# Optimization experiments

Measured on AMD Instinct MI355X. Metric: run time of the kernel, lower is better.

Reference implementation:

```python
import jax, jax.numpy as jnp
import numpy as np

B, H, S, D = 2, 16, 2048, 64
SCALE = D ** -0.5  # head_dim^-0.5 with dim=1024, num_heads=16


def setup_inputs() -> dict:
    key = jax.random.key(0)
    kq, kk, kv = jax.random.split(key, 3)
    q = jax.random.normal(kq, (B, H, S, D), dtype=jnp.float32)
    k = jax.random.normal(kk, (B, H, S, D), dtype=jnp.float32)
    v = jax.random.normal(kv, (B, H, S, D), dtype=jnp.float32)
    # causal mask, broadcastable over batch and heads; 0 -> masked
    mask = jnp.tril(jnp.ones((S, S), dtype=jnp.int32))[None, None]
    return {"q": q, "k": k, "v": v, "mask": mask}


def reference(q, k, v, mask):
    # scores: [B, H, S, S]
    scores = jnp.einsum("bhqd,bhkd->bhqk", q, k) * SCALE
    scores = jnp.where(mask == 0, jnp.float32(-jnp.inf), scores)
    attn_weights = jax.nn.softmax(scores, axis=-1)
    # dropout p=0 / eval mode -> identity
    attn_output = jnp.einsum("bhqk,bhkd->bhqd", attn_weights, v)
    return attn_output, attn_weights
```

## Files before the change

kernel.cpp:

```cpp
#include <hip/hip_runtime.h>


#define S_LEN 2048
#define HD 64
#define NHEADS 32
#define NQT 32
#define ATT_SCALE 0.125f

typedef __bf16 bf16x8 __attribute__((ext_vector_type(8)));
typedef unsigned short u16x8 __attribute__((ext_vector_type(8)));
typedef float f32x4 __attribute__((ext_vector_type(4)));

__device__ __forceinline__ unsigned short f2bf(float f) {
  unsigned int u = __builtin_bit_cast(unsigned int, f);
  u += 0x7fffu + ((u >> 16) & 1u);
  return (unsigned short)(u >> 16);
}
__device__ __forceinline__ bf16x8 frag16(const unsigned short* p) {
  uint4 u = *reinterpret_cast<const uint4*>(p);
  return __builtin_bit_cast(bf16x8, u);
}
__device__ __forceinline__ bf16x8 cvt8(const float* p) {
  const float4 a = *reinterpret_cast<const float4*>(p);
  const float4 b = *reinterpret_cast<const float4*>(p + 4);
  u16x8 r;
  r[0] = f2bf(a.x); r[1] = f2bf(a.y); r[2] = f2bf(a.z); r[3] = f2bf(a.w);
  r[4] = f2bf(b.x); r[5] = f2bf(b.y); r[6] = f2bf(b.z); r[7] = f2bf(b.w);
  return __builtin_bit_cast(bf16x8, r);
}
__device__ __forceinline__ bf16x8 load8(const void* base, size_t off, bool isf32) {
  if (isf32) return cvt8(reinterpret_cast<const float*>(base) + off);
  return frag16(reinterpret_cast<const unsigned short*>(base) + off);
}
__device__ __forceinline__ bool sniff_f32(const void* q) {
  const int lane = threadIdx.x & 63;
  const unsigned int w = reinterpret_cast<const unsigned int*>(q)[lane];
  const unsigned int le = (w >> 7) & 0xFFu;
  const bool okb = (le == 0u) || (le >= 100u && le <= 140u);
  return __popcll(__ballot(okb)) < 32;
}

__global__ __launch_bounds__(256) void prep_kernel(
    const void* __restrict__ q, const void* __restrict__ k, const void* __restrict__ v,
    unsigned short* __restrict__ wq, unsigned short* __restrict__ wk,
    unsigned short* __restrict__ wv) {
  __shared__ __align__(16) unsigned short T[HD][72];
  const int tid = threadIdx.x;
  if (blockIdx.x >= 1024) {
    const bool isf32 = sniff_f32(q);
    const size_t i = ((size_t)(blockIdx.x - 1024) * 256 + tid) * 8;
    bf16x8 a = load8(q, i, isf32);
    *reinterpret_cast<uint4*>(wq + i) = __builtin_bit_cast(uint4, a);
    bf16x8 b = load8(k, i, isf32);
    *reinterpret_cast<uint4*>(wk + i) = __builtin_bit_cast(uint4, b);
    return;
  }
  const bool isf32 = sniff_f32(v);
  const int head = blockIdx.x & (NHEADS - 1);
  const int tt = blockIdx.x >> 5;
  const int r = tid >> 2;
  const int dc = (tid & 3) << 4;
  const size_t off = ((size_t)head * S_LEN + (tt << 6) + r) * HD + dc;
  const bf16x8 x0 = load8(v, off, isf32);
  const bf16x8 x1 = load8(v, off + 8, isf32);
  const u16x8 e0 = __builtin_bit_cast(u16x8, x0);
  const u16x8 e1 = __builtin_bit_cast(u16x8, x1);
#pragma unroll
  for (int e = 0; e < 8; ++e) { T[dc + e][r] = e0[e]; T[dc + 8 + e][r] = e1[e]; }
  __syncthreads();
  const int d = tid >> 2;
  const int tc = (tid & 3) << 4;
  const uint4 o0 = *reinterpret_cast<const uint4*>(&T[d][tc]);
  const uint4 o1 = *reinterpret_cast<const uint4*>(&T[d][tc + 8]);
  unsigned short* dst = wv + ((size_t)head * HD + d) * S_LEN + (tt << 6) + tc;
  *reinterpret_cast<uint4*>(dst) = o0;
  *reinterpret_cast<uint4*>(dst + 8) = o1;
}

template <bool WS>
__global__ __launch_bounds__(256, 4) void attn_kernel(
    const void* __restrict__ q, const void* __restrict__ kk, const void* __restrict__ vv,
    const unsigned short* __restrict__ wq, const unsigned short* __restrict__ wk,
    const unsigned short* __restrict__ wv,
    float* __restrict__ out_o, float* __restrict__ out_w) {
  __shared__ __align__(16) unsigned short Vt[2][HD * 72];
  __shared__ __align__(16) unsigned short Pt[4][16 * 72];

  const int blk = blockIdx.x;
  const int head = blk & (NHEADS - 1);
  const int qt = (NQT - 1) - (blk >> 5);
  const int tid = threadIdx.x;
  const int lane = tid & 63;
  const int wave = tid >> 6;
  const int q0 = qt << 6;
  const int r0 = q0 + (wave << 4);
  const int l15 = lane & 15;
  const int quad = lane >> 4;

  bool isf32 = true;
  if constexpr (!WS) isf32 = sniff_f32(q);

  const size_t qb = (size_t)head * S_LEN * HD;
  float* Wh = out_w + (size_t)head * S_LEN * S_LEN;

  {
    const int c0 = (qt + 1) << 6;
    const int nz4 = (S_LEN - c0) >> 2;
    const int row = tid >> 2;
    const f32x4 z = {0.f, 0.f, 0.f, 0.f};
    f32x4* wrow = reinterpret_cast<f32x4*>(Wh + (size_t)(q0 + row) * S_LEN + c0);
    for (int c = tid & 3; c < nz4; c += 4) __builtin_nontemporal_store(z, wrow + c);
  }

  const size_t qoff = qb + (size_t)(r0 + l15) * HD + (quad << 3);
  bf16x8 qa0, qa1;
  if constexpr (WS) { qa0 = frag16(wq + qoff); qa1 = frag16(wq + qoff + 32); }
  else              { qa0 = load8(q, qoff, isf32); qa1 = load8(q, qoff + 32, isf32); }

  auto ldk = [&](int kt, int f) -> bf16x8 {
    const size_t o = qb + (size_t)((kt << 6) + ((f >> 1) << 4) + l15) * HD +
                     (quad << 3) + ((f & 1) << 5);
    if constexpr (WS) return frag16(wk + o);
    else return load8(kk, o, isf32);
  };

  bf16x8 kc[8], kn[8];

  float lsum[4] = {0.f, 0.f, 0.f, 0.f};
#pragma unroll
  for (int f = 0; f < 8; ++f) kc[f] = ldk(0, f);
  for (int kt = 0; kt <= qt; ++kt) {
    if (kt < qt) {
#pragma unroll
      for (int f = 0; f < 8; ++f) kn[f] = ldk(kt + 1, f);
    }
    if (kt == qt) {
#pragma unroll
      for (int nc = 0; nc < 4; ++nc) {
        f32x4 acc = {0.f, 0.f, 0.f, 0.f};
        acc = __builtin_amdgcn_mfma_f32_16x16x32_bf16(qa0, kc[2 * nc], acc, 0, 0, 0);
        acc = __builtin_amdgcn_mfma_f32_16x16x32_bf16(qa1, kc[2 * nc + 1], acc, 0, 0, 0);
        const int ki = (kt << 6) + (nc << 4) + l15;
#pragma unroll
        for (int r = 0; r < 4; ++r) {
          const int qi = r0 + (quad << 2) + r;
          lsum[r] += (ki <= qi) ? __expf(acc[r] * ATT_SCALE) : 0.f;
        }
      }
    } else {
#pragma unroll
      for (int nc = 0; nc < 4; ++nc) {
        f32x4 acc = {0.f, 0.f, 0.f, 0.f};
        acc = __builtin_amdgcn_mfma_f32_16x16x32_bf16(qa0, kc[2 * nc], acc, 0, 0, 0);
        acc = __builtin_amdgcn_mfma_f32_16x16x32_bf16(qa1, kc[2 * nc + 1], acc, 0, 0, 0);
#pragma unroll
        for (int r = 0; r < 4; ++r) lsum[r] += __expf(acc[r] * ATT_SCALE);
      }
#pragma unroll
      for (int f = 0; f < 8; ++f) kc[f] = kn[f];
    }
  }
  float inv_l[4];
#pragma unroll
  for (int r = 0; r < 4; ++r) {
    float s = lsum[r];
    s += __shfl_xor(s, 1);
    s += __shfl_xor(s, 2);
    s += __shfl_xor(s, 4);
    s += __shfl_xor(s, 8);
    inv_l[r] = 1.0f / s;
  }

  const f32x4 vzero = {0.f, 0.f, 0.f, 0.f};
  f32x4 oacc[4] = {vzero, vzero, vzero, vzero};
  unsigned short* Pw = &Pt[wave][0];

  const int vd1 = tid >> 3, vtb1 = tid & 7;
  const int vd2 = (tid + 256) >> 3, vtb2 = tid & 7;
  const unsigned short* wvh = wv + (size_t)head * HD * S_LEN;
  const int ftr1 = tid >> 3, fdc = (tid & 7) << 3;
  const int ftr2 = (tid + 256) >> 3;

  uint4 va0, va1;
  bf16x8 fv0, fv1;

  auto vload = [&](int kt) {
    if constexpr (WS) {
      const unsigned short* b = wvh + (kt << 6);
      va0 = *reinterpret_cast<const uint4*>(b + (size_t)vd1 * S_LEN + (vtb1 << 3));
      va1 = *reinterpret_cast<const uint4*>(b + (size_t)vd2 * S_LEN + (vtb2 << 3));
    } else {
      fv0 = load8(vv, qb + (size_t)((kt << 6) + ftr1) * HD + fdc, isf32);
      fv1 = load8(vv, qb + (size_t)((kt << 6) + ftr2) * HD + fdc, isf32);
    }
  };
  auto vstage = [&](int buf) {
    if constexpr (WS) {
      *reinterpret_cast<uint4*>(&Vt[buf][vd1 * 72 + ((vtb1 ^ (vd1 >> 3)) << 3)]) = va0;
      *reinterpret_cast<uint4*>(&Vt[buf][vd2 * 72 + ((vtb2 ^ (vd2 >> 3)) << 3)]) = va1;
    } else {
      const u16x8 s0 = __builtin_bit_cast(u16x8, fv0);
      const u16x8 s1 = __builtin_bit_cast(u16x8, fv1);
      const int tb1 = ftr1 >> 3, tl1 = ftr1 & 7;
      const int tb2 = ftr2 >> 3, tl2 = ftr2 & 7;
#pragma unroll
      for (int e = 0; e < 8; ++e) {
        const int d = fdc + e;
        Vt[buf][d * 72 + (((tb1 ^ (d >> 3)) << 3) | tl1)] = s0[e];
        Vt[buf][d * 72 + (((tb2 ^ (d >> 3)) << 3) | tl2)] = s1[e];
      }
    }
  };

#pragma unroll
  for (int f = 0; f < 8; ++f) kc[f] = ldk(0, f);
  vload(0);
  vstage(0);
  __syncthreads();

  for (int kt = 0; kt <= qt; ++kt) {
    const bool last = (kt == qt);
    if (!last) {
#pragma unroll
      for (int f = 0; f < 8; ++f) kn[f] = ldk(kt + 1, f);
      vload(kt + 1);
    }

#pragma unroll
    for (int nc = 0; nc < 4; ++nc) {
      f32x4 acc = {0.f, 0.f, 0.f, 0.f};
      acc = __builtin_amdgcn_mfma_f32_16x16x32_bf16(qa0, kc[2 * nc], acc, 0, 0, 0);
      acc = __builtin_amdgcn_mfma_f32_16x16x32_bf16(qa1, kc[2 * nc + 1], acc, 0, 0, 0);
      const int ki = (kt << 6) + (nc << 4) + l15;
#pragma unroll
      for (int r = 0; r < 4; ++r) {
        const int qi = r0 + (quad << 2) + r;
        float p = __expf(acc[r] * ATT_SCALE) * inv_l[r];
        if (last) p = (ki <= qi) ? p : 0.f;
        __builtin_nontemporal_store(p, &Wh[(size_t)(r0 + (quad << 2) + r) * S_LEN + ki]);
        Pw[((quad << 2) + r) * 72 + (nc << 4) + l15] = f2bf(p);
      }
    }

    {
      const bf16x8 pa0 = frag16(Pw + l15 * 72 + (quad << 3));
      const bf16x8 pa1 = frag16(Pw + l15 * 72 + 32 + (quad << 3));
      const unsigned short* Vc = &Vt[kt & 1][0];
#pragma unroll
      for (int nc2 = 0; nc2 < 4; ++nc2) {
        const int n = (nc2 << 4) + l15;
        const unsigned short* vbp = Vc + n * 72;
        const int nb = n >> 3;
        const bf16x8 v0 = frag16(vbp + ((quad ^ nb) << 3));
        const bf16x8 v1 = frag16(vbp + (((4 + quad) ^ nb) << 3));
        oacc[nc2] = __builtin_amdgcn_mfma_f32_16x16x32_bf16(pa0, v0, oacc[nc2], 0, 0, 0);
        oacc[nc2] = __builtin_amdgcn_mfma_f32_16x16x32_bf16(pa1, v1, oacc[nc2], 0, 0, 0);
      }
    }

    if (!last) {
      vstage((kt + 1) & 1);
      __syncthreads();
#pragma unroll
      for (int f = 0; f < 8; ++f) kc[f] = kn[f];
    }
  }

#pragma unroll
  for (int nc2 = 0; nc2 < 4; ++nc2)
#pragma unroll
    for (int r = 0; r < 4; ++r)
      out_o[(size_t)(head * S_LEN + r0 + (quad << 2) + r) * HD + (nc2 << 4) + l15] =
          oacc[nc2][r];
}

extern "C" void kernel_launch(void* const* d_in, const int* in_sizes, int n_in,
                              void* d_out, int out_size, void* d_ws, size_t ws_size,
                              hipStream_t stream) {
  (void)in_sizes; (void)n_in; (void)out_size;
  const void* q = d_in[0];
  const void* k = d_in[1];
  const void* v = d_in[2];
  float* out = (float*)d_out;
  float* out_o = out;
  float* out_w = out + (size_t)NHEADS * S_LEN * HD;
  const size_t NE = (size_t)NHEADS * S_LEN * HD;
  if (d_ws && ws_size >= NE * 2 * 3) {
    unsigned short* wq = reinterpret_cast<unsigned short*>(d_ws);
    unsigned short* wk = wq + NE;
    unsigned short* wv = wk + NE;
    prep_kernel<<<dim3(1024 + NE / (256 * 8)), dim3(256), 0, stream>>>(q, k, v, wq, wk, wv);
    attn_kernel<true><<<dim3(NHEADS * NQT), dim3(256), 0, stream>>>(
        q, k, v, wq, wk, wv, out_o, out_w);
  } else {
    attn_kernel<false><<<dim3(NHEADS * NQT), dim3(256), 0, stream>>>(
        q, k, v, nullptr, nullptr, nullptr, out_o, out_w);
  }
}
```

Measured before the change: 762.1 us.

## Compute transposed scores to keep P in registers and drop LDS staging

The QK^T MFMA is swapped to compute S^T, and the K rows are permuted so that each lane's accumulator outputs line up directly with the A-operand layout of the PV MFMA. This removes the per-wave LDS round trip for P. In the workspace path V is pre-transposed into per-tile 64x64 blocks and read straight from global memory, which removes the shared V buffer and the per-tile __syncthreads. Attention-weight stores become 16-byte vector nontemporal stores, and the row-sum reduction shrinks to one scalar with two shuffles. In exchange, K prefetching across iterations is dropped and V fragment loads now hit global memory or cache every tile, which can expose load latency.

```diff
diff --git a/kernel.cpp b/kernel.cpp
--- a/kernel.cpp
+++ b/kernel.cpp
@@ -72,7 +72,7 @@
   const int tc = (tid & 3) << 4;
   const uint4 o0 = *reinterpret_cast<const uint4*>(&T[d][tc]);
   const uint4 o1 = *reinterpret_cast<const uint4*>(&T[d][tc + 8]);
-  unsigned short* dst = wv + ((size_t)head * HD + d) * S_LEN + (tt << 6) + tc;
+  unsigned short* dst = wv + (((size_t)(head * NQT + tt) * HD + d) << 6) + tc;
   *reinterpret_cast<uint4*>(dst) = o0;
   *reinterpret_cast<uint4*>(dst + 8) = o1;
 }
@@ -83,8 +83,7 @@
     const unsigned short* __restrict__ wq, const unsigned short* __restrict__ wk,
     const unsigned short* __restrict__ wv,
     float* __restrict__ out_o, float* __restrict__ out_w) {
-  __shared__ __align__(16) unsigned short Vt[2][HD * 72];
-  __shared__ __align__(16) unsigned short Pt[4][16 * 72];
+  __shared__ __align__(16) unsigned short Vt[WS ? 8 : 2 * HD * 72];
 
   const int blk = blockIdx.x;
   const int head = blk & (NHEADS - 1);
@@ -117,135 +116,167 @@
   if constexpr (WS) { qa0 = frag16(wq + qoff); qa1 = frag16(wq + qoff + 32); }
   else              { qa0 = load8(q, qoff, isf32); qa1 = load8(q, qoff + 32, isf32); }
 
+  const int krow_l = ((l15 >> 2) << 3) + (l15 & 3);
   auto ldk = [&](int kt, int f) -> bf16x8 {
-    const size_t o = qb + (size_t)((kt << 6) + ((f >> 1) << 4) + l15) * HD +
-                     (quad << 3) + ((f & 1) << 5);
+    const int s = f >> 1;
+    const int row = (kt << 6) + krow_l + ((s & 1) << 2) + ((s >> 1) << 5);
+    const size_t o = qb + (size_t)row * HD + (quad << 3) + ((f & 1) << 5);
     if constexpr (WS) return frag16(wk + o);
     else return load8(kk, o, isf32);
   };
-
-  bf16x8 kc[8], kn[8];
-
-  float lsum[4] = {0.f, 0.f, 0.f, 0.f};
-#pragma unroll
-  for (int f = 0; f < 8; ++f) kc[f] = ldk(0, f);
-  for (int kt = 0; kt <= qt; ++kt) {
-    if (kt < qt) {
-#pragma unroll
-      for (int f = 0; f < 8; ++f) kn[f] = ldk(kt + 1, f);
+  const int kib_base = (quad << 3);
+  const int qi = r0 + l15;
+
+  float lsum = 0.f;
+  {
+    bf16x8 kc[8], kn[8];
+#pragma unroll
+    for (int f = 0; f < 8; ++f) kc[f] = ldk(0, f);
+    for (int kt = 0; kt <= qt; ++kt) {
+      if (kt < qt) {
+#pragma unroll
+        for (int f = 0; f < 8; ++f) kn[f] = ldk(kt + 1, f);
+      }
+      if (kt == qt) {
+#pragma unroll
+        for (int s = 0; s < 4; ++s) {
+          f32x4 acc = {0.f, 0.f, 0.f, 0.f};
+          acc = __builtin_amdgcn_mfma_f32_16x16x32_bf16(kc[2 * s], qa0, acc, 0, 0, 0);
+          acc = __builtin_amdgcn_mfma_f32_16x16x32_bf16(kc[2 * s + 1], qa1, acc, 0, 0, 0);
+          const int kib = (kt << 6) + kib_base + ((s & 1) << 2) + ((s >> 1) << 5);
+#pragma unroll
+          for (int r = 0; r < 4; ++r)
+            lsum += (kib + r <= qi) ? __expf(acc[r] * ATT_SCALE) : 0.f;
+        }
+      } else {
+#pragma unroll
+        for (int s = 0; s < 4; ++s) {
+          f32x4 acc = {0.f, 0.f, 0.f, 0.f};
+          acc = __builtin_amdgcn_mfma_f32_16x16x32_bf16(kc[2 * s], qa0, acc, 0, 0, 0);
+          acc = __builtin_amdgcn_mfma_f32_16x16x32_bf16(kc[2 * s + 1], qa1, acc, 0, 0, 0);
+#pragma unroll
+          for (int r = 0; r < 4; ++r) lsum += __expf(acc[r] * ATT_SCALE);
+        }
+#pragma unroll
+        for (int f = 0; f < 8; ++f) kc[f] = kn[f];
+      }
     }
-    if (kt == qt) {
-#pragma unroll
-      for (int nc = 0; nc < 4; ++nc) {
-        f32x4 acc = {0.f, 0.f, 0.f, 0.f};
-        acc = __builtin_amdgcn_mfma_f32_16x16x32_bf16(qa0, kc[2 * nc], acc, 0, 0, 0);
-        acc = __builtin_amdgcn_mfma_f32_16x16x32_bf16(qa1, kc[2 * nc + 1], acc, 0, 0, 0);
-        const int ki = (kt << 6) + (nc << 4) + l15;
-#pragma unroll
-        for (int r = 0; r < 4; ++r) {
-          const int qi = r0 + (quad << 2) + r;
-          lsum[r] += (ki <= qi) ? __expf(acc[r] * ATT_SCALE) : 0.f;
-        }
-      }
-    } else {
-#pragma unroll
-      for (int nc = 0; nc < 4; ++nc) {
-        f32x4 acc = {0.f, 0.f, 0.f, 0.f};
-        acc = __builtin_amdgcn_mfma_f32_16x16x32_bf16(qa0, kc[2 * nc], acc, 0, 0, 0);
-        acc = __builtin_amdgcn_mfma_f32_16x16x32_bf16(qa1, kc[2 * nc + 1], acc, 0, 0, 0);
-#pragma unroll
-        for (int r = 0; r < 4; ++r) lsum[r] += __expf(acc[r] * ATT_SCALE);
-      }
-#pragma unroll
-      for (int f = 0; f < 8; ++f) kc[f] = kn[f];
-    }
-  }
-  float inv_l[4];
-#pragma unroll
-  for (int r = 0; r < 4; ++r) {
-    float s = lsum[r];
-    s += __shfl_xor(s, 1);
-    s += __shfl_xor(s, 2);
-    s += __shfl_xor(s, 4);
-    s += __shfl_xor(s, 8);
-    inv_l[r] = 1.0f / s;
-  }
+  }
+  lsum += __shfl_xor(lsum, 16);
+  lsum += __shfl_xor(lsum, 32);
+  const float inv_l = 1.0f / lsum;
 
   const f32x4 vzero = {0.f, 0.f, 0.f, 0.f};
   f32x4 oacc[4] = {vzero, vzero, vzero, vzero};
-  unsigned short* Pw = &Pt[wave][0];
-
-  const int vd1 = tid >> 3, vtb1 = tid & 7;
-  const int vd2 = (tid + 256) >> 3, vtb2 = tid & 7;
-  const unsigned short* wvh = wv + (size_t)head * HD * S_LEN;
-  const int ftr1 = tid >> 3, fdc = (tid & 7) << 3;
-  const int ftr2 = (tid + 256) >> 3;
-
-  uint4 va0, va1;
-  bf16x8 fv0, fv1;
-
-  auto vload = [&](int kt) {
-    if constexpr (WS) {
-      const unsigned short* b = wvh + (kt << 6);
-      va0 = *reinterpret_cast<const uint4*>(b + (size_t)vd1 * S_LEN + (vtb1 << 3));
-      va1 = *reinterpret_cast<const uint4*>(b + (size_t)vd2 * S_LEN + (vtb2 << 3));
-    } else {
+
+  if constexpr (WS) {
+    const unsigned short* wvh = wv + ((size_t)(head * NQT) << 12);
+    for (int kt = 0; kt <= qt; ++kt) {
+      const bool last = (kt == qt);
+      bf16x8 kf[8];
+#pragma unroll
+      for (int f = 0; f < 8; ++f) kf[f] = ldk(kt, f);
+      bf16x8 vf[8];
+      {
+        const unsigned short* tb = wvh + ((size_t)kt << 12);
+#pragma unroll
+        for (int nc2 = 0; nc2 < 4; ++nc2) {
+          const unsigned short* rp = tb + (((nc2 << 4) + l15) << 6) + (quad << 3);
+          vf[2 * nc2] = frag16(rp);
+          vf[2 * nc2 + 1] = frag16(rp + 32);
+        }
+      }
+
+      float pb[4][4];
+#pragma unroll
+      for (int s = 0; s < 4; ++s) {
+        f32x4 acc = {0.f, 0.f, 0.f, 0.f};
+        acc = __builtin_amdgcn_mfma_f32_16x16x32_bf16(kf[2 * s], qa0, acc, 0, 0, 0);
+        acc = __builtin_amdgcn_mfma_f32_16x16x32_bf16(kf[2 * s + 1], qa1, acc, 0, 0, 0);
+        const int kib = (kt << 6) + kib_base + ((s & 1) << 2) + ((s >> 1) << 5);
+        f32x4 pv;
+#pragma unroll
+        for (int r = 0; r < 4; ++r) {
+          float p = __expf(acc[r] * ATT_SCALE) * inv_l;
+          if (last) p = (kib + r <= qi) ? p : 0.f;
+          pb[s][r] = p;
+          pv[r] = p;
+        }
+        __builtin_nontemporal_store(
+            pv, reinterpret_cast<f32x4*>(Wh + (size_t)qi * S_LEN + kib));
+      }
+      u16x8 a0, a1;
+#pragma unroll
+      for (int r = 0; r < 4; ++r) {
+        a0[r] = f2bf(pb[0][r]); a0[4 + r] = f2bf(pb[1][r]);
+        a1[r] = f2bf(pb[2][r]); a1[4 + r] = f2bf(pb[3][r]);
+      }
+      const bf16x8 pa0 = __builtin_bit_cast(bf16x8, a0);
+      const bf16x8 pa1 = __builtin_bit_cast(bf16x8, a1);
+#pragma unroll
+      for (int nc2 = 0; nc2 < 4; ++nc2) {
+        oacc[nc2] = __builtin_amdgcn_mfma_f32_16x16x32_bf16(pa0, vf[2 * nc2], oacc[nc2], 0, 0, 0);
+        oacc[nc2] = __builtin_amdgcn_mfma_f32_16x16x32_bf16(pa1, vf[2 * nc2 + 1], oacc[nc2], 0, 0, 0);
+      }
+    }
+  } else {
+    const int ftr1 = tid >> 3, fdc = (tid & 7) << 3;
+    const int ftr2 = (tid + 256) >> 3;
+    bf16x8 fv0, fv1;
+    auto vload = [&](int kt) {
       fv0 = load8(vv, qb + (size_t)((kt << 6) + ftr1) * HD + fdc, isf32);
       fv1 = load8(vv, qb + (size_t)((kt << 6) + ftr2) * HD + fdc, isf32);
-    }
-  };
-  auto vstage = [&](int buf) {
-    if constexpr (WS) {
-      *reinterpret_cast<uint4*>(&Vt[buf][vd1 * 72 + ((vtb1 ^ (vd1 >> 3)) << 3)]) = va0;
-      *reinterpret_cast<uint4*>(&Vt[buf][vd2 * 72 + ((vtb2 ^ (vd2 >> 3)) << 3)]) = va1;
-    } else {
+    };
+    auto vstage = [&](int buf) {
       const u16x8 s0 = __builtin_bit_cast(u16x8, fv0);
       const u16x8 s1 = __builtin_bit_cast(u16x8, fv1);
       const int tb1 = ftr1 >> 3, tl1 = ftr1 & 7;
       const int tb2 = ftr2 >> 3, tl2 = ftr2 & 7;
+      unsigned short* Vb = &Vt[buf * HD * 72];
 #pragma unroll
       for (int e = 0; e < 8; ++e) {
         const int d = fdc + e;
-        Vt[buf][d * 72 + (((tb1 ^ (d >> 3)) << 3) | tl1)] = s0[e];
-        Vt[buf][d * 72 + (((tb2 ^ (d >> 3)) << 3) | tl2)] = s1[e];
-      }
-    }
-  };
-
-#pragma unroll
-  for (int f = 0; f < 8; ++f) kc[f] = ldk(0, f);
-  vload(0);
-  vstage(0);
-  __syncthreads();
-
-  for (int kt = 0; kt <= qt; ++kt) {
-    const bool last = (kt == qt);
-    if (!last) {
-#pragma unroll
-      for (int f = 0; f < 8; ++f) kn[f] = ldk(kt + 1, f);
-      vload(kt + 1);
-    }
-
-#pragma unroll
-    for (int nc = 0; nc < 4; ++nc) {
-      f32x4 acc = {0.f, 0.f, 0.f, 0.f};
-      acc = __builtin_amdgcn_mfma_f32_16x16x32_bf16(qa0, kc[2 * nc], acc, 0, 0, 0);
-      acc = __builtin_amdgcn_mfma_f32_16x16x32_bf16(qa1, kc[2 * nc + 1], acc, 0, 0, 0);
-      const int ki = (kt << 6) + (nc << 4) + l15;
+        Vb[d * 72 + (((tb1 ^ (d >> 3)) << 3) | tl1)] = s0[e];
+        Vb[d * 72 + (((tb2 ^ (d >> 3)) << 3) | tl2)] = s1[e];
+      }
+    };
+    vload(0);
+    vstage(0);
+    __syncthreads();
+    for (int kt = 0; kt <= qt; ++kt) {
+      const bool last = (kt == qt);
+      bf16x8 kf[8];
+#pragma unroll
+      for (int f = 0; f < 8; ++f) kf[f] = ldk(kt, f);
+      if (!last) vload(kt + 1);
+
+      float pb[4][4];
+#pragma unroll
+      for (int s = 0; s < 4; ++s) {
+        f32x4 acc = {0.f, 0.f, 0.f, 0.f};
+        acc = __builtin_amdgcn_mfma_f32_16x16x32_bf16(kf[2 * s], qa0, acc, 0, 0, 0);
+        acc = __builtin_amdgcn_mfma_f32_16x16x32_bf16(kf[2 * s + 1], qa1, acc, 0, 0, 0);
+        const int kib = (kt << 6) + kib_base + ((s & 1) << 2) + ((s >> 1) << 5);
+        f32x4 pv;
+#pragma unroll
+        for (int r = 0; r < 4; ++r) {
+          float p = __expf(acc[r] * ATT_SCALE) * inv_l;
+          if (last) p = (kib + r <= qi) ? p : 0.f;
+          pb[s][r] = p;
+          pv[r] = p;
+        }
+        __builtin_nontemporal_store(
+            pv, reinterpret_cast<f32x4*>(Wh + (size_t)qi * S_LEN + kib));
+      }
+      u16x8 a0, a1;
 #pragma unroll
       for (int r = 0; r < 4; ++r) {
-        const int qi = r0 + (quad << 2) + r;
-        float p = __expf(acc[r] * ATT_SCALE) * inv_l[r];
-        if (last) p = (ki <= qi) ? p : 0.f;
-        __builtin_nontemporal_store(p, &Wh[(size_t)(r0 + (quad << 2) + r) * S_LEN + ki]);
-        Pw[((quad << 2) + r) * 72 + (nc << 4) + l15] = f2bf(p);
-      }
-    }
-
-    {
-      const bf16x8 pa0 = frag16(Pw + l15 * 72 + (quad << 3));
-      const bf16x8 pa1 = frag16(Pw + l15 * 72 + 32 + (quad << 3));
-      const unsigned short* Vc = &Vt[kt & 1][0];
+        a0[r] = f2bf(pb[0][r]); a0[4 + r] = f2bf(pb[1][r]);
+        a1[r] = f2bf(pb[2][r]); a1[4 + r] = f2bf(pb[3][r]);
+      }
+      const bf16x8 pa0 = __builtin_bit_cast(bf16x8, a0);
+      const bf16x8 pa1 = __builtin_bit_cast(bf16x8, a1);
+      const unsigned short* Vc = &Vt[(kt & 1) * HD * 72];
 #pragma unroll
       for (int nc2 = 0; nc2 < 4; ++nc2) {
         const int n = (nc2 << 4) + l15;
@@ -256,13 +287,10 @@
         oacc[nc2] = __builtin_amdgcn_mfma_f32_16x16x32_bf16(pa0, v0, oacc[nc2], 0, 0, 0);
         oacc[nc2] = __builtin_amdgcn_mfma_f32_16x16x32_bf16(pa1, v1, oacc[nc2], 0, 0, 0);
       }
-    }
-
-    if (!last) {
-      vstage((kt + 1) & 1);
-      __syncthreads();
-#pragma unroll
-      for (int f = 0; f < 8; ++f) kc[f] = kn[f];
+      if (!last) {
+        vstage((kt + 1) & 1);
+        __syncthreads();
+      }
     }
   }
 
```

Result: slower. 779.6 us (+2.3%).
